# Performance work log

Hardware: AMD Instinct MI355X
Metric: run time of the kernel (lower is better)

## Reference

```python
import jax, jax.numpy as jnp
import numpy as np

MORA_DIV = 2


def setup_inputs() -> dict:
    key = jax.random.key(0)
    k1, k2, k3, k4 = jax.random.split(key, 4)
    d = 4096
    m = d // MORA_DIV
    x = jax.random.normal(k1, (4, 2048, d), dtype=jnp.float32)
    weight = jax.random.normal(k2, (d, d), dtype=jnp.float32) * 0.02
    mora = jax.random.normal(k3, (m, m), dtype=jnp.float32) * 0.02
    # dora_mag initialized as column L2 norm of the frozen weight (1, d_in)
    dora_mag = jnp.linalg.norm(weight, axis=0, keepdims=True)
    return {"x": x, "weight": weight, "mora": mora, "dora_mag": dora_mag}


def reference(x, weight, mora, dora_mag):
    # Tile the small adapter into full (d_out, d_in): repeat_interleave on both dims
    adapter = jnp.repeat(jnp.repeat(mora, MORA_DIV, axis=0), MORA_DIV, axis=1)
    w = weight + adapter                      # (d_out, d_in)
    col_norm = jnp.linalg.norm(w, axis=0, keepdims=True)  # (1, d_in)
    w = dora_mag * (w / col_norm)             # DoRA magnitude rescale
    return jnp.einsum('bsd,od->bso', x, w)    # F.linear, no bias
```

## Files before the change

### kernel.cpp

```cpp
#include <hip/hip_runtime.h>
#include <stdint.h>

#define M_TOT 8192
#define N_TOT 4096
#define K_TOT 4096
#define BM 256
#define BN 256
#define BK 32
#define NT (K_TOT / BK)

typedef short  s16x8 __attribute__((ext_vector_type(8)));
typedef unsigned short u16x8 __attribute__((ext_vector_type(8)));
typedef float  f32x4 __attribute__((ext_vector_type(4)));

__device__ __forceinline__ unsigned short f32_to_bf16(float f) {
  union { float f; unsigned u; } v; v.f = f;
  unsigned r = v.u + 0x7FFFu + ((v.u >> 16) & 1u);
  return (unsigned short)(r >> 16);
}

__device__ __forceinline__ void gload_lds16(void* lds, const void* g) {
  __builtin_amdgcn_global_load_lds(
      (const __attribute__((address_space(1))) unsigned int*)g,
      (__attribute__((address_space(3))) unsigned int*)lds,
      16, 0, 0);
}

__global__ void colnorm_partial_k(const float* __restrict__ weight,
                                  const float* __restrict__ mora,
                                  float* __restrict__ partials) {
  int d = blockIdx.x * 256 + threadIdx.x;
  int o0 = blockIdx.y * 128;
  float s = 0.f;
  #pragma unroll 4
  for (int o = o0; o < o0 + 128; ++o) {
    float w = weight[(size_t)o * K_TOT + d] + mora[(size_t)(o >> 1) * 2048 + (d >> 1)];
    s = fmaf(w, w, s);
  }
  partials[blockIdx.y * K_TOT + d] = s;
}

__global__ void scale_k(const float* __restrict__ partials,
                        const float* __restrict__ dora_mag,
                        float* __restrict__ scale) {
  int d = blockIdx.x * 256 + threadIdx.x;
  float s = 0.f;
  #pragma unroll
  for (int c = 0; c < 32; ++c) s += partials[c * K_TOT + d];
  scale[d] = dora_mag[d] / sqrtf(s);
}

__global__ void pack_w_k(const float* __restrict__ weight,
                         const float* __restrict__ mora,
                         const float* __restrict__ scale,
                         unsigned short* __restrict__ wb) {
  size_t idx = ((size_t)blockIdx.x * 256 + threadIdx.x) * 8;
  int o = (int)(idx >> 12);
  int d = (int)(idx & (K_TOT - 1));
  float4 w0 = *(const float4*)(weight + idx);
  float4 w1 = *(const float4*)(weight + idx + 4);
  float4 mv = *(const float4*)(mora + (size_t)(o >> 1) * 2048 + (d >> 1));
  float4 s0 = *(const float4*)(scale + d);
  float4 s1 = *(const float4*)(scale + d + 4);
  u16x8 r;
  r[0] = f32_to_bf16((w0.x + mv.x) * s0.x);
  r[1] = f32_to_bf16((w0.y + mv.x) * s0.y);
  r[2] = f32_to_bf16((w0.z + mv.y) * s0.z);
  r[3] = f32_to_bf16((w0.w + mv.y) * s0.w);
  r[4] = f32_to_bf16((w1.x + mv.z) * s1.x);
  r[5] = f32_to_bf16((w1.y + mv.z) * s1.y);
  r[6] = f32_to_bf16((w1.z + mv.w) * s1.z);
  r[7] = f32_to_bf16((w1.w + mv.w) * s1.w);
  *(u16x8*)(wb + idx) = r;
}

__global__ void pack_x_k(const float* __restrict__ x, unsigned short* __restrict__ xb) {
  size_t idx = ((size_t)blockIdx.x * 256 + threadIdx.x) * 8;
  float4 v0 = *(const float4*)(x + idx);
  float4 v1 = *(const float4*)(x + idx + 4);
  u16x8 r;
  r[0] = f32_to_bf16(v0.x); r[1] = f32_to_bf16(v0.y);
  r[2] = f32_to_bf16(v0.z); r[3] = f32_to_bf16(v0.w);
  r[4] = f32_to_bf16(v1.x); r[5] = f32_to_bf16(v1.y);
  r[6] = f32_to_bf16(v1.z); r[7] = f32_to_bf16(v1.w);
  *(u16x8*)(xb + idx) = r;
}

__global__ void __launch_bounds__(512, 2) gemm_bf16_k(
    const unsigned short* __restrict__ xb,
    const unsigned short* __restrict__ wb,
    float* __restrict__ out) {
  __shared__ short lds[4][2][BM * BK];

  const int tid = threadIdx.x;
  const int l   = tid & 63;
  const int wid = tid >> 6;
  const int wm  = wid >> 2;
  const int wn  = wid & 3;

  const int orig = blockIdx.x;
  const int swz  = (orig & 7) * (512 >> 3) + (orig >> 3);
  const int by = swz >> 4;
  const int bx = swz & 15;

  const unsigned short* ag = xb + (size_t)(by * BM) * K_TOT;
  const unsigned short* bg = wb + (size_t)(bx * BN) * K_TOT;

  const int c0 = tid, c1 = 512 + tid;
  const int r0s = c0 >> 2, r1s = c1 >> 2;
  const int g0 = (c0 & 3) ^ ((r0s >> 1) & 3);
  const int g1 = (c1 & 3) ^ ((r1s >> 1) & 3);
  const unsigned short* gA0 = ag + (size_t)r0s * K_TOT + g0 * 8;
  const unsigned short* gA1 = ag + (size_t)r1s * K_TOT + g1 * 8;
  const unsigned short* gB0 = bg + (size_t)r0s * K_TOT + g0 * 8;
  const unsigned short* gB1 = bg + (size_t)r1s * K_TOT + g1 * 8;
  const int lo0 = (tid & ~63) * 8;
  const int lo1 = lo0 + 512 * 8;

  const int lrow = l & 15;
  const int key  = (lrow >> 1) & 3;
  const int blk  = ((l >> 4) ^ key) * 8;
  const int aoffb = (wm * 128 + lrow) * BK + blk;
  const int boffb = (wn * 64  + lrow) * BK + blk;

  s16x8 afr[4], bfr[4];
  f32x4 acc[8][4] = {};

#define STG_A(t) { short* p = &lds[(t) & 3][0][0]; \
    gload_lds16(p + lo0, gA0 + (size_t)(t) * BK); \
    gload_lds16(p + lo1, gA1 + (size_t)(t) * BK); }
#define STG_B(t) { short* p = &lds[(t) & 3][1][0]; \
    gload_lds16(p + lo0, gB0 + (size_t)(t) * BK); \
    gload_lds16(p + lo1, gB1 + (size_t)(t) * BK); }
#define DS_A(t, mb) { const short* p = &lds[(t) & 3][0][aoffb + (mb) * 16 * BK]; \
    afr[0] = *(const s16x8*)(p);               afr[1] = *(const s16x8*)(p + 16 * BK); \
    afr[2] = *(const s16x8*)(p + 32 * BK);     afr[3] = *(const s16x8*)(p + 48 * BK); }
#define DS_B(t) { const short* p = &lds[(t) & 3][1][boffb]; \
    bfr[0] = *(const s16x8*)(p);               bfr[1] = *(const s16x8*)(p + 16 * BK); \
    bfr[2] = *(const s16x8*)(p + 32 * BK);     bfr[3] = *(const s16x8*)(p + 48 * BK); }
#define BAR() __builtin_amdgcn_s_barrier()
#define LGKM0() asm volatile("s_waitcnt lgkmcnt(0)" ::: "memory")
#define VM8() asm volatile("s_waitcnt vmcnt(8)" ::: "memory")
#define VM4() asm volatile("s_waitcnt vmcnt(4)" ::: "memory")
#define VM0() asm volatile("s_waitcnt vmcnt(0)" ::: "memory")
#define MM(mb) { __builtin_amdgcn_s_setprio(1); \
    _Pragma("unroll") for (int mm = 0; mm < 4; ++mm) { \
      _Pragma("unroll") for (int nn = 0; nn < 4; ++nn) \
        acc[(mb) + mm][nn] = __builtin_amdgcn_mfma_f32_16x16x32_bf16(afr[mm], bfr[nn], acc[(mb) + mm][nn], 0, 0, 0); } \
    __builtin_amdgcn_s_setprio(0); }

  STG_A(0); STG_B(0); STG_A(1); STG_B(1); STG_A(2); STG_B(2);
  VM8(); BAR();

  #pragma unroll 1
  for (int t = 0; t < NT - 4; t += 2) {
    DS_A(t, 0); DS_B(t);
    STG_A(t + 3);
    BAR(); LGKM0(); MM(0); BAR();
    DS_A(t, 4);
    STG_B(t + 3);
    BAR(); LGKM0(); MM(4);
    VM8(); BAR();
    DS_A(t + 1, 0); DS_B(t + 1);
    STG_A(t + 4);
    BAR(); LGKM0(); MM(0); BAR();
    DS_A(t + 1, 4);
    STG_B(t + 4);
    BAR(); LGKM0(); MM(4);
    VM8(); BAR();
  }

  DS_A(124, 0); DS_B(124);
  STG_A(127);
  BAR(); LGKM0(); MM(0); BAR();
  DS_A(124, 4);
  STG_B(127);
  BAR(); LGKM0(); MM(4);
  VM8(); BAR();
  DS_A(125, 0); DS_B(125);
  BAR(); LGKM0(); MM(0); BAR();
  DS_A(125, 4);
  BAR(); LGKM0(); MM(4);
  VM4(); BAR();
  DS_A(126, 0); DS_B(126);
  BAR(); LGKM0(); MM(0); BAR();
  DS_A(126, 4);
  BAR(); LGKM0(); MM(4);
  VM0(); BAR();
  DS_A(127, 0); DS_B(127);
  BAR(); LGKM0(); MM(0); BAR();
  DS_A(127, 4);
  LGKM0(); MM(4);

#undef STG_A
#undef STG_B
#undef DS_A
#undef DS_B
#undef MM

  const int row0 = by * BM + wm * 128 + (l >> 4) * 4;
  const int col0 = bx * BN + wn * 64 + lrow;
  #pragma unroll
  for (int m = 0; m < 8; ++m)
    #pragma unroll
    for (int n = 0; n < 4; ++n) {
      #pragma unroll
      for (int j = 0; j < 4; ++j)
        out[(size_t)(row0 + m * 16 + j) * N_TOT + col0 + n * 16] = acc[m][n][j];
    }
}

__global__ void gemm_fb_k(const float* __restrict__ x, const float* __restrict__ weight,
                          const float* __restrict__ mora, const float* __restrict__ scale,
                          float* __restrict__ out) {
  __shared__ float As[64][17];
  __shared__ float Bs[64][17];
  int t = threadIdx.x;
  int bx = blockIdx.x, by = blockIdx.y;
  int tr = t >> 4, tc = t & 15;
  float c[4][4] = {};
  for (int kt = 0; kt < K_TOT; kt += 16) {
    #pragma unroll
    for (int r = 0; r < 4; ++r) {
      int idx = r * 256 + t;
      int row = idx >> 4, col = idx & 15;
      As[row][col] = x[(size_t)(by * 64 + row) * K_TOT + kt + col];
      int o = bx * 64 + row, d = kt + col;
      Bs[row][col] = (weight[(size_t)o * K_TOT + d] + mora[(size_t)(o >> 1) * 2048 + (d >> 1)]) * scale[d];
    }
    __syncthreads();
    #pragma unroll
    for (int k = 0; k < 16; ++k) {
      float av[4], bv[4];
      #pragma unroll
      for (int i = 0; i < 4; ++i) av[i] = As[tr * 4 + i][k];
      #pragma unroll
      for (int j = 0; j < 4; ++j) bv[j] = Bs[tc * 4 + j][k];
      #pragma unroll
      for (int i = 0; i < 4; ++i)
        #pragma unroll
        for (int j = 0; j < 4; ++j)
          c[i][j] = fmaf(av[i], bv[j], c[i][j]);
    }
    __syncthreads();
  }
  #pragma unroll
  for (int i = 0; i < 4; ++i)
    #pragma unroll
    for (int j = 0; j < 4; ++j)
      out[(size_t)(by * 64 + tr * 4 + i) * N_TOT + bx * 64 + tc * 4 + j] = c[i][j];
}

extern "C" void kernel_launch(void* const* d_in, const int* in_sizes, int n_in,
                              void* d_out, int out_size, void* d_ws, size_t ws_size,
                              hipStream_t stream) {
  const float* x      = (const float*)d_in[0];
  const float* weight = (const float*)d_in[1];
  const float* mora   = (const float*)d_in[2];
  const float* dora   = (const float*)d_in[3];
  float* out = (float*)d_out;

  char* ws = (char*)d_ws;
  float* partials = (float*)ws;
  float* scale    = (float*)(ws + (512 << 10));
  const size_t OFF_W = (size_t)1 << 20;
  unsigned short* wbuf = (unsigned short*)(ws + OFF_W);
  unsigned short* xbuf = (unsigned short*)(ws + OFF_W + (size_t)N_TOT * K_TOT * 2);
  const size_t NEED = OFF_W + (size_t)N_TOT * K_TOT * 2 + (size_t)M_TOT * K_TOT * 2;

  dim3 b256(256);
  colnorm_partial_k<<<dim3(16, 32), b256, 0, stream>>>(weight, mora, partials);
  scale_k<<<16, b256, 0, stream>>>(partials, dora, scale);

  if (ws_size >= NEED) {
    pack_w_k<<<(N_TOT * K_TOT) / (256 * 8), b256, 0, stream>>>(weight, mora, scale, wbuf);
    pack_x_k<<<(M_TOT * K_TOT) / (256 * 8), b256, 0, stream>>>(x, xbuf);
    gemm_bf16_k<<<(M_TOT / BM) * (N_TOT / BN), 512, 0, stream>>>(xbuf, wbuf, out);
  } else {
    gemm_fb_k<<<dim3(N_TOT / 64, M_TOT / 64), b256, 0, stream>>>(x, weight, mora, scale, out);
  }
}
```

Baseline: 324.8 us.

## Double-buffer register fragments to overlap LDS reads with MFMA compute

Restructures the GEMM main loop so full A/B fragments for the next K-tile are read from LDS into a second register set while MFMAs run on the current set. This cuts the barriers per K-step from four to one and merges the A/B global-to-LDS staging into a single macro. The aim is to hide LDS read latency and barrier stalls behind matrix math. It roughly doubles fragment register usage (24 vs 8 vectors), which may raise register pressure and lower occupancy, and sched_barrier fences limit how freely the compiler can reorder.

Result: no change. 323.6 us (-0.4%).

```diff
diff --git a/kernel.cpp b/kernel.cpp
--- a/kernel.cpp
+++ b/kernel.cpp
@@ -123,80 +123,69 @@
   const int aoffb = (wm * 128 + lrow) * BK + blk;
   const int boffb = (wn * 64  + lrow) * BK + blk;
 
-  s16x8 afr[4], bfr[4];
+  s16x8 af0[8], bf0[4], af1[8], bf1[4];
   f32x4 acc[8][4] = {};
 
-#define STG_A(t) { short* p = &lds[(t) & 3][0][0]; \
-    gload_lds16(p + lo0, gA0 + (size_t)(t) * BK); \
-    gload_lds16(p + lo1, gA1 + (size_t)(t) * BK); }
-#define STG_B(t) { short* p = &lds[(t) & 3][1][0]; \
-    gload_lds16(p + lo0, gB0 + (size_t)(t) * BK); \
-    gload_lds16(p + lo1, gB1 + (size_t)(t) * BK); }
-#define DS_A(t, mb) { const short* p = &lds[(t) & 3][0][aoffb + (mb) * 16 * BK]; \
-    afr[0] = *(const s16x8*)(p);               afr[1] = *(const s16x8*)(p + 16 * BK); \
-    afr[2] = *(const s16x8*)(p + 32 * BK);     afr[3] = *(const s16x8*)(p + 48 * BK); }
-#define DS_B(t) { const short* p = &lds[(t) & 3][1][boffb]; \
-    bfr[0] = *(const s16x8*)(p);               bfr[1] = *(const s16x8*)(p + 16 * BK); \
-    bfr[2] = *(const s16x8*)(p + 32 * BK);     bfr[3] = *(const s16x8*)(p + 48 * BK); }
+#define STG(t) { \
+    short* pa = &lds[(t) & 3][0][0]; short* pb = &lds[(t) & 3][1][0]; \
+    gload_lds16(pa + lo0, gA0 + (size_t)(t) * BK); \
+    gload_lds16(pb + lo0, gB0 + (size_t)(t) * BK); \
+    gload_lds16(pa + lo1, gA1 + (size_t)(t) * BK); \
+    gload_lds16(pb + lo1, gB1 + (size_t)(t) * BK); }
+#define READF(t, af, bf) { \
+    const short* pa = &lds[(t) & 3][0][aoffb]; \
+    const short* pb = &lds[(t) & 3][1][boffb]; \
+    _Pragma("unroll") for (int i = 0; i < 4; ++i) bf[i] = *(const s16x8*)(pb + i * 16 * BK); \
+    _Pragma("unroll") for (int i = 0; i < 8; ++i) af[i] = *(const s16x8*)(pa + i * 16 * BK); }
+#define MMAF(af, bf) { __builtin_amdgcn_s_setprio(1); \
+    _Pragma("unroll") for (int mm = 0; mm < 8; ++mm) { \
+      _Pragma("unroll") for (int nn = 0; nn < 4; ++nn) \
+        acc[mm][nn] = __builtin_amdgcn_mfma_f32_16x16x32_bf16(af[mm], bf[nn], acc[mm][nn], 0, 0, 0); } \
+    __builtin_amdgcn_s_setprio(0); }
 #define BAR() __builtin_amdgcn_s_barrier()
+#define SB0() __builtin_amdgcn_sched_barrier(0)
 #define LGKM0() asm volatile("s_waitcnt lgkmcnt(0)" ::: "memory")
 #define VM8() asm volatile("s_waitcnt vmcnt(8)" ::: "memory")
 #define VM4() asm volatile("s_waitcnt vmcnt(4)" ::: "memory")
 #define VM0() asm volatile("s_waitcnt vmcnt(0)" ::: "memory")
-#define MM(mb) { __builtin_amdgcn_s_setprio(1); \
-    _Pragma("unroll") for (int mm = 0; mm < 4; ++mm) { \
-      _Pragma("unroll") for (int nn = 0; nn < 4; ++nn) \
-        acc[(mb) + mm][nn] = __builtin_amdgcn_mfma_f32_16x16x32_bf16(afr[mm], bfr[nn], acc[(mb) + mm][nn], 0, 0, 0); } \
-    __builtin_amdgcn_s_setprio(0); }
-
-  STG_A(0); STG_B(0); STG_A(1); STG_B(1); STG_A(2); STG_B(2);
-  VM8(); BAR();
+
+  STG(0); STG(1); STG(2);
+  VM8(); BAR(); SB0();
+  READF(0, af0, bf0);
 
   #pragma unroll 1
   for (int t = 0; t < NT - 4; t += 2) {
-    DS_A(t, 0); DS_B(t);
-    STG_A(t + 3);
-    BAR(); LGKM0(); MM(0); BAR();
-    DS_A(t, 4);
-    STG_B(t + 3);
-    BAR(); LGKM0(); MM(4);
-    VM8(); BAR();
-    DS_A(t + 1, 0); DS_B(t + 1);
-    STG_A(t + 4);
-    BAR(); LGKM0(); MM(0); BAR();
-    DS_A(t + 1, 4);
-    STG_B(t + 4);
-    BAR(); LGKM0(); MM(4);
-    VM8(); BAR();
-  }
-
-  DS_A(124, 0); DS_B(124);
-  STG_A(127);
-  BAR(); LGKM0(); MM(0); BAR();
-  DS_A(124, 4);
-  STG_B(127);
-  BAR(); LGKM0(); MM(4);
-  VM8(); BAR();
-  DS_A(125, 0); DS_B(125);
-  BAR(); LGKM0(); MM(0); BAR();
-  DS_A(125, 4);
-  BAR(); LGKM0(); MM(4);
-  VM4(); BAR();
-  DS_A(126, 0); DS_B(126);
-  BAR(); LGKM0(); MM(0); BAR();
-  DS_A(126, 4);
-  BAR(); LGKM0(); MM(4);
-  VM0(); BAR();
-  DS_A(127, 0); DS_B(127);
-  BAR(); LGKM0(); MM(0); BAR();
-  DS_A(127, 4);
-  LGKM0(); MM(4);
-
-#undef STG_A
-#undef STG_B
-#undef DS_A
-#undef DS_B
-#undef MM
+    STG(t + 3);
+    VM8(); LGKM0(); BAR(); SB0();
+    READF(t + 1, af1, bf1);
+    SB0();
+    MMAF(af0, bf0);
+    STG(t + 4);
+    VM8(); LGKM0(); BAR(); SB0();
+    READF(t + 2, af0, bf0);
+    SB0();
+    MMAF(af1, bf1);
+  }
+
+  STG(127);
+  VM8(); LGKM0(); BAR(); SB0();
+  READF(125, af1, bf1);
+  SB0();
+  MMAF(af0, bf0);
+  VM4(); LGKM0(); BAR(); SB0();
+  READF(126, af0, bf0);
+  SB0();
+  MMAF(af1, bf1);
+  VM0(); LGKM0(); BAR(); SB0();
+  READF(127, af1, bf1);
+  SB0();
+  MMAF(af0, bf0);
+  LGKM0();
+  MMAF(af1, bf1);
+
+#undef STG
+#undef READF
+#undef MMAF
 
   const int row0 = by * BM + wm * 128 + (l >> 4) * 4;
   const int col0 = bx * BN + wn * 64 + lrow;
```
